# Optimization experiments

Hardware: AMD Instinct MI355X
Metric: run time of the kernel (lower is better)

Reference implementation:

```python
import jax, jax.numpy as jnp
import numpy as np

NUM_HEADS = 4
SCALE = 0.17677669529663687  # head_dim**-0.5, head_dim=32


def setup_inputs() -> dict:
    key = jax.random.key(0)
    k1, k2 = jax.random.split(key)
    qkv = jax.random.normal(k1, (2048, 144, 384), dtype=jnp.float32)
    mask = jax.random.normal(k2, (1, NUM_HEADS, 144, 144), dtype=jnp.float32)
    return {"qkv": qkv, "mask": mask}


def reference(qkv, mask):
    B, N, C = qkv.shape
    head_dim = C // NUM_HEADS // 3
    # [B,N,3,H,d] -> [3,B,H,N,d]
    qkv = qkv.reshape(B, N, 3, NUM_HEADS, head_dim).transpose(2, 0, 3, 1, 4)
    q, k, v = qkv[0], qkv[1], qkv[2]
    q = q * SCALE
    attn = jnp.einsum('bhnd,bhmd->bhnm', q, k) + mask  # mask broadcasts over B
    attn = jax.nn.softmax(attn, axis=-1)
    out = jnp.einsum('bhnm,bhmd->bhnd', attn, v)  # [B,H,N,d]
    return out.transpose(0, 2, 1, 3).reshape(B, N, C // 3)
```

## Files before the change

### kernel.cpp

```cpp
#include <hip/hip_runtime.h>


using short8 = __attribute__((ext_vector_type(8))) short;
using f32x4  = __attribute__((ext_vector_type(4))) float;

#define SEQ   144
#define NH    4
#define HD    32
#define C3    384
#define OC    128

#define KSTR  56
#define VSTR  168
#define PSTR  168

#define LOG2E 1.4426950408889634f
#define SCALE 0.17677669529663687f

__device__ __forceinline__ unsigned short f2bf(float f) {
  unsigned int u = __float_as_uint(f);
  u += 0x7fffu + ((u >> 16) & 1u);
  return (unsigned short)(u >> 16);
}

__global__ __launch_bounds__(256, 3)
void attn_kernel(const float* __restrict__ qkv,
                 const float* __restrict__ mask,
                 float* __restrict__ out)
{
  __shared__ __align__(16) unsigned short sK [SEQ * KSTR];
  __shared__ __align__(16) unsigned short sVT[HD  * VSTR];
  __shared__ __align__(16) unsigned short sP [4][16 * PSTR];

  const int tid = threadIdx.x;
  const int bid = blockIdx.x;
  const int b = bid >> 2;
  const int h = bid & 3;

  const float* qbase = qkv + (size_t)b * (SEQ * C3) + h * HD;
  const float* kbase = qbase + NH * HD;
  const float* vbase = qbase + 2 * NH * HD;

  {
    const int n0 = tid >> 4;
    const int d2 = (tid & 15) * 2;
    for (int p = 0; p < 9; ++p) {
      int n = p * 16 + n0;
      float2 kv = *(const float2*)(kbase + (size_t)n * C3 + d2);
      unsigned int pk = (unsigned int)f2bf(kv.x) | ((unsigned int)f2bf(kv.y) << 16);
      *(unsigned int*)&sK[n * KSTR + d2] = pk;
    }
  }
  {
    const int d  = tid & 31;
    const int n0 = tid >> 5;
    for (int p = 0; p < 18; ++p) {
      int n = p * 8 + n0;
      float v = vbase[(size_t)n * C3 + d];
      sVT[d * VSTR + n] = f2bf(v);
    }
    const int r  = tid >> 3;
    const int c0 = tid & 7;
    for (int p = 0; p < 3; ++p)
      sVT[r * VSTR + 144 + c0 + p * 8] = 0;
  }
  __syncthreads();

  const int lane = tid & 63;
  const int wv   = tid >> 6;
  const int m    = lane & 15;
  const int quad = lane >> 4;

  unsigned short* pbuf = sP[wv];
  for (int i = 0; i < 4; ++i) {
    int e = lane * 4 + i;
    pbuf[(e >> 4) * PSTR + 144 + (e & 15)] = 0;
  }

  const float qs = SCALE * LOG2E;
  const float* mbase = mask + (size_t)h * SEQ * SEQ;

  for (int s = wv; s < 9; s += 4) {
    short8 afrag;
    {
      const float* qrow = qbase + (size_t)(s * 16 + m) * C3 + quad * 8;
      float4 q0 = *(const float4*)(qrow);
      float4 q1 = *(const float4*)(qrow + 4);
      afrag[0] = (short)f2bf(q0.x * qs); afrag[1] = (short)f2bf(q0.y * qs);
      afrag[2] = (short)f2bf(q0.z * qs); afrag[3] = (short)f2bf(q0.w * qs);
      afrag[4] = (short)f2bf(q1.x * qs); afrag[5] = (short)f2bf(q1.y * qs);
      afrag[6] = (short)f2bf(q1.z * qs); afrag[7] = (short)f2bf(q1.w * qs);
    }

    float S[9][4];
    for (int nt = 0; nt < 9; ++nt) {
      f32x4 c = {0.f, 0.f, 0.f, 0.f};
      short8 bfrag = *(const short8*)&sK[(nt * 16 + m) * KSTR + quad * 8];
      c = __builtin_amdgcn_mfma_f32_16x16x32_bf16(afrag, bfrag, c, 0, 0, 0);
      const float* mrow = mbase + (size_t)(s * 16 + quad * 4) * SEQ + nt * 16 + m;
      S[nt][0] = c[0] + mrow[0 * SEQ] * LOG2E;
      S[nt][1] = c[1] + mrow[1 * SEQ] * LOG2E;
      S[nt][2] = c[2] + mrow[2 * SEQ] * LOG2E;
      S[nt][3] = c[3] + mrow[3 * SEQ] * LOG2E;
    }

    float mx[4], l[4];
    for (int r = 0; r < 4; ++r) {
      float v = S[0][r];
      for (int nt = 1; nt < 9; ++nt) v = fmaxf(v, S[nt][r]);
      v = fmaxf(v, __shfl_xor(v, 1));
      v = fmaxf(v, __shfl_xor(v, 2));
      v = fmaxf(v, __shfl_xor(v, 4));
      v = fmaxf(v, __shfl_xor(v, 8));
      mx[r] = v;
      l[r] = 0.f;
    }
    for (int nt = 0; nt < 9; ++nt)
      for (int r = 0; r < 4; ++r) {
        float p = __builtin_amdgcn_exp2f(S[nt][r] - mx[r]);
        S[nt][r] = p;
        l[r] += p;
      }
    for (int r = 0; r < 4; ++r) {
      float v = l[r];
      v += __shfl_xor(v, 1);
      v += __shfl_xor(v, 2);
      v += __shfl_xor(v, 4);
      v += __shfl_xor(v, 8);
      l[r] = 1.0f / v;
    }

    for (int nt = 0; nt < 9; ++nt)
      for (int r = 0; r < 4; ++r)
        pbuf[(quad * 4 + r) * PSTR + nt * 16 + m] = f2bf(S[nt][r]);

    f32x4 acc0 = {0.f, 0.f, 0.f, 0.f}, acc1 = {0.f, 0.f, 0.f, 0.f};
    for (int kt = 0; kt < 5; ++kt) {
      short8 pa = *(const short8*)&pbuf[m * PSTR + kt * 32 + quad * 8];
      short8 b0 = *(const short8*)&sVT[(m)      * VSTR + kt * 32 + quad * 8];
      short8 b1 = *(const short8*)&sVT[(16 + m) * VSTR + kt * 32 + quad * 8];
      acc0 = __builtin_amdgcn_mfma_f32_16x16x32_bf16(pa, b0, acc0, 0, 0, 0);
      acc1 = __builtin_amdgcn_mfma_f32_16x16x32_bf16(pa, b1, acc1, 0, 0, 0);
    }

    float* orow = out + ((size_t)b * SEQ + s * 16 + quad * 4) * OC + h * HD + m;
    for (int r = 0; r < 4; ++r) {
      orow[r * OC]      = acc0[r] * l[r];
      orow[r * OC + 16] = acc1[r] * l[r];
    }
  }
}

extern "C" void kernel_launch(void* const* d_in, const int* in_sizes, int n_in,
                              void* d_out, int out_size, void* d_ws, size_t ws_size,
                              hipStream_t stream) {
  const float* qkv  = (const float*)d_in[0];
  const float* mask = (const float*)d_in[1];
  float* out = (float*)d_out;
  attn_kernel<<<dim3(2048 * NH), dim3(256), 0, stream>>>(qkv, mask, out);
}
```

Measured before the change: 653.2 us.

## Vectorize K/V staging, prescale mask, swap PV operands for float4 stores

Loads K and V as float4 in one combined staging loop and packs bf16 with the library conversion. Q fragments are loaded before the staging barrier. A small pre-kernel multiplies the mask by log2e into the workspace, so it can serve directly as the MFMA accumulator init. The PV product now has V as the A operand, which makes each lane own contiguous output columns and allows float4 stores. It also trims the padded K tile with a half-masked final MFMA, shrinks LDS strides, and raises launch bounds to 4 blocks per CU. The cost is an extra kernel launch and different LDS bank patterns from the new strides.

```diff
diff --git a/kernel.cpp b/kernel.cpp
--- a/kernel.cpp
+++ b/kernel.cpp
@@ -1,4 +1,5 @@
 #include <hip/hip_runtime.h>
+#include <hip/hip_bf16.h>
 
 
 using short8 = __attribute__((ext_vector_type(8))) short;
@@ -10,9 +11,9 @@
 #define C3    384
 #define OC    128
 
-#define KSTR  56
-#define VSTR  168
-#define PSTR  168
+#define KSTR  40
+#define VSTR  152
+#define PSTR  152
 
 #define LOG2E 1.4426950408889634f
 #define SCALE 0.17677669529663687f
@@ -22,15 +23,25 @@
   u += 0x7fffu + ((u >> 16) & 1u);
   return (unsigned short)(u >> 16);
 }
-
-__global__ __launch_bounds__(256, 3)
+__device__ __forceinline__ unsigned int pkbf(float a, float b) {
+  __hip_bfloat162 h = __float22bfloat162_rn(make_float2(a, b));
+  union { __hip_bfloat162 h2; unsigned int u; } cv; cv.h2 = h;
+  return cv.u;
+}
+
+__global__ void mask_prep(const float* __restrict__ mask, float* __restrict__ o) {
+  int i = blockIdx.x * 256 + threadIdx.x;
+  o[i] = mask[i] * LOG2E;
+}
+
+__global__ __launch_bounds__(256, 4)
 void attn_kernel(const float* __restrict__ qkv,
-                 const float* __restrict__ mask,
+                 const float* __restrict__ maskS,
                  float* __restrict__ out)
 {
+  __shared__ __align__(16) unsigned short sP [4 * 16 * PSTR];
+  __shared__ __align__(16) unsigned short sVT[HD * VSTR];
   __shared__ __align__(16) unsigned short sK [SEQ * KSTR];
-  __shared__ __align__(16) unsigned short sVT[HD  * VSTR];
-  __shared__ __align__(16) unsigned short sP [4][16 * PSTR];
 
   const int tid = threadIdx.x;
   const int bid = blockIdx.x;
@@ -41,112 +52,147 @@
   const float* kbase = qbase + NH * HD;
   const float* vbase = qbase + 2 * NH * HD;
 
-  {
-    const int n0 = tid >> 4;
-    const int d2 = (tid & 15) * 2;
-    for (int p = 0; p < 9; ++p) {
-      int n = p * 16 + n0;
-      float2 kv = *(const float2*)(kbase + (size_t)n * C3 + d2);
-      unsigned int pk = (unsigned int)f2bf(kv.x) | ((unsigned int)f2bf(kv.y) << 16);
-      *(unsigned int*)&sK[n * KSTR + d2] = pk;
-    }
-  }
-  {
-    const int d  = tid & 31;
-    const int n0 = tid >> 5;
-    for (int p = 0; p < 18; ++p) {
-      int n = p * 8 + n0;
-      float v = vbase[(size_t)n * C3 + d];
-      sVT[d * VSTR + n] = f2bf(v);
-    }
-    const int r  = tid >> 3;
-    const int c0 = tid & 7;
-    for (int p = 0; p < 3; ++p)
-      sVT[r * VSTR + 144 + c0 + p * 8] = 0;
-  }
-  __syncthreads();
-
   const int lane = tid & 63;
   const int wv   = tid >> 6;
   const int m    = lane & 15;
   const int quad = lane >> 4;
 
-  unsigned short* pbuf = sP[wv];
-  for (int i = 0; i < 4; ++i) {
-    int e = lane * 4 + i;
-    pbuf[(e >> 4) * PSTR + 144 + (e & 15)] = 0;
-  }
-
   const float qs = SCALE * LOG2E;
-  const float* mbase = mask + (size_t)h * SEQ * SEQ;
-
-  for (int s = wv; s < 9; s += 4) {
-    short8 afrag;
-    {
+  float4 q0[3], q1[3];
+#pragma unroll
+  for (int i = 0; i < 3; ++i) {
+    int s = wv + 4 * i;
+    if (s < 9) {
       const float* qrow = qbase + (size_t)(s * 16 + m) * C3 + quad * 8;
-      float4 q0 = *(const float4*)(qrow);
-      float4 q1 = *(const float4*)(qrow + 4);
-      afrag[0] = (short)f2bf(q0.x * qs); afrag[1] = (short)f2bf(q0.y * qs);
-      afrag[2] = (short)f2bf(q0.z * qs); afrag[3] = (short)f2bf(q0.w * qs);
-      afrag[4] = (short)f2bf(q1.x * qs); afrag[5] = (short)f2bf(q1.y * qs);
-      afrag[6] = (short)f2bf(q1.z * qs); afrag[7] = (short)f2bf(q1.w * qs);
+      q0[i] = *(const float4*)(qrow);
+      q1[i] = *(const float4*)(qrow + 4);
     }
-
-    float S[9][4];
-    for (int nt = 0; nt < 9; ++nt) {
-      f32x4 c = {0.f, 0.f, 0.f, 0.f};
-      short8 bfrag = *(const short8*)&sK[(nt * 16 + m) * KSTR + quad * 8];
-      c = __builtin_amdgcn_mfma_f32_16x16x32_bf16(afrag, bfrag, c, 0, 0, 0);
-      const float* mrow = mbase + (size_t)(s * 16 + quad * 4) * SEQ + nt * 16 + m;
-      S[nt][0] = c[0] + mrow[0 * SEQ] * LOG2E;
-      S[nt][1] = c[1] + mrow[1 * SEQ] * LOG2E;
-      S[nt][2] = c[2] + mrow[2 * SEQ] * LOG2E;
-      S[nt][3] = c[3] + mrow[3 * SEQ] * LOG2E;
-    }
-
-    float mx[4], l[4];
-    for (int r = 0; r < 4; ++r) {
-      float v = S[0][r];
-      for (int nt = 1; nt < 9; ++nt) v = fmaxf(v, S[nt][r]);
-      v = fmaxf(v, __shfl_xor(v, 1));
-      v = fmaxf(v, __shfl_xor(v, 2));
-      v = fmaxf(v, __shfl_xor(v, 4));
-      v = fmaxf(v, __shfl_xor(v, 8));
-      mx[r] = v;
-      l[r] = 0.f;
-    }
-    for (int nt = 0; nt < 9; ++nt)
+  }
+
+  const int nr = tid >> 3;
+  const int d4 = (tid & 7) * 4;
+#pragma unroll
+  for (int p = 0; p < 4; ++p) {
+    int n = p * 32 + nr;
+    float4 k4 = *(const float4*)(kbase + (size_t)n * C3 + d4);
+    unsigned long long w = (unsigned long long)pkbf(k4.x, k4.y)
+                         | ((unsigned long long)pkbf(k4.z, k4.w) << 32);
+    *(unsigned long long*)&sK[n * KSTR + d4] = w;
+    float4 v4 = *(const float4*)(vbase + (size_t)n * C3 + d4);
+    sVT[(d4 + 0) * VSTR + n] = f2bf(v4.x);
+    sVT[(d4 + 1) * VSTR + n] = f2bf(v4.y);
+    sVT[(d4 + 2) * VSTR + n] = f2bf(v4.z);
+    sVT[(d4 + 3) * VSTR + n] = f2bf(v4.w);
+  }
+  if (nr < 16) {
+    int n = 128 + nr;
+    float4 k4 = *(const float4*)(kbase + (size_t)n * C3 + d4);
+    unsigned long long w = (unsigned long long)pkbf(k4.x, k4.y)
+                         | ((unsigned long long)pkbf(k4.z, k4.w) << 32);
+    *(unsigned long long*)&sK[n * KSTR + d4] = w;
+    float4 v4 = *(const float4*)(vbase + (size_t)n * C3 + d4);
+    sVT[(d4 + 0) * VSTR + n] = f2bf(v4.x);
+    sVT[(d4 + 1) * VSTR + n] = f2bf(v4.y);
+    sVT[(d4 + 2) * VSTR + n] = f2bf(v4.z);
+    sVT[(d4 + 3) * VSTR + n] = f2bf(v4.w);
+  }
+  __syncthreads();
+
+  unsigned short* pbuf = sP + wv * (16 * PSTR);
+  const float* mb = maskS + (size_t)h * SEQ * SEQ;
+
+#pragma unroll
+  for (int i = 0; i < 3; ++i) {
+    int s = wv + 4 * i;
+    if (s < 9) {
+      union { short8 s8; unsigned int u[4]; } af;
+      af.u[0] = pkbf(q0[i].x * qs, q0[i].y * qs);
+      af.u[1] = pkbf(q0[i].z * qs, q0[i].w * qs);
+      af.u[2] = pkbf(q1[i].x * qs, q1[i].y * qs);
+      af.u[3] = pkbf(q1[i].z * qs, q1[i].w * qs);
+
+      float S[9][4];
+      const float* mrow0 = mb + (size_t)(s * 16 + quad * 4) * SEQ + m;
+#pragma unroll
+      for (int nt = 0; nt < 9; ++nt) {
+        const float* mr = mrow0 + nt * 16;
+        f32x4 c;
+        c[0] = mr[0]; c[1] = mr[SEQ]; c[2] = mr[2 * SEQ]; c[3] = mr[3 * SEQ];
+        short8 bfrag = *(const short8*)&sK[(nt * 16 + m) * KSTR + quad * 8];
+        c = __builtin_amdgcn_mfma_f32_16x16x32_bf16(af.s8, bfrag, c, 0, 0, 0);
+        S[nt][0] = c[0]; S[nt][1] = c[1]; S[nt][2] = c[2]; S[nt][3] = c[3];
+      }
+
+      float mx[4], l[4];
+#pragma unroll
       for (int r = 0; r < 4; ++r) {
-        float p = __builtin_amdgcn_exp2f(S[nt][r] - mx[r]);
-        S[nt][r] = p;
-        l[r] += p;
-      }
-    for (int r = 0; r < 4; ++r) {
-      float v = l[r];
-      v += __shfl_xor(v, 1);
-      v += __shfl_xor(v, 2);
-      v += __shfl_xor(v, 4);
-      v += __shfl_xor(v, 8);
-      l[r] = 1.0f / v;
-    }
-
-    for (int nt = 0; nt < 9; ++nt)
-      for (int r = 0; r < 4; ++r)
-        pbuf[(quad * 4 + r) * PSTR + nt * 16 + m] = f2bf(S[nt][r]);
-
-    f32x4 acc0 = {0.f, 0.f, 0.f, 0.f}, acc1 = {0.f, 0.f, 0.f, 0.f};
-    for (int kt = 0; kt < 5; ++kt) {
-      short8 pa = *(const short8*)&pbuf[m * PSTR + kt * 32 + quad * 8];
-      short8 b0 = *(const short8*)&sVT[(m)      * VSTR + kt * 32 + quad * 8];
-      short8 b1 = *(const short8*)&sVT[(16 + m) * VSTR + kt * 32 + quad * 8];
-      acc0 = __builtin_amdgcn_mfma_f32_16x16x32_bf16(pa, b0, acc0, 0, 0, 0);
-      acc1 = __builtin_amdgcn_mfma_f32_16x16x32_bf16(pa, b1, acc1, 0, 0, 0);
-    }
-
-    float* orow = out + ((size_t)b * SEQ + s * 16 + quad * 4) * OC + h * HD + m;
-    for (int r = 0; r < 4; ++r) {
-      orow[r * OC]      = acc0[r] * l[r];
-      orow[r * OC + 16] = acc1[r] * l[r];
+        float a = fmaxf(fmaxf(S[0][r], S[1][r]), S[2][r]);
+        float bb = fmaxf(fmaxf(S[3][r], S[4][r]), S[5][r]);
+        float cc = fmaxf(fmaxf(S[6][r], S[7][r]), S[8][r]);
+        float v = fmaxf(fmaxf(a, bb), cc);
+        v = fmaxf(v, __shfl_xor(v, 1));
+        v = fmaxf(v, __shfl_xor(v, 2));
+        v = fmaxf(v, __shfl_xor(v, 4));
+        v = fmaxf(v, __shfl_xor(v, 8));
+        mx[r] = v; l[r] = 0.f;
+      }
+#pragma unroll
+      for (int nt = 0; nt < 9; ++nt)
+#pragma unroll
+        for (int r = 0; r < 4; ++r) {
+          float p = __builtin_amdgcn_exp2f(S[nt][r] - mx[r]);
+          S[nt][r] = p;
+          l[r] += p;
+        }
+#pragma unroll
+      for (int r = 0; r < 4; ++r) {
+        float v = l[r];
+        v += __shfl_xor(v, 1);
+        v += __shfl_xor(v, 2);
+        v += __shfl_xor(v, 4);
+        v += __shfl_xor(v, 8);
+        l[r] = v;
+      }
+      int src = (m >> 2) * 16 + m;
+      float s0 = __shfl(l[0], src), s1 = __shfl(l[1], src);
+      float s2 = __shfl(l[2], src), s3 = __shfl(l[3], src);
+      float lsel = (m & 2) ? ((m & 1) ? s3 : s2) : ((m & 1) ? s1 : s0);
+      float linv = __builtin_amdgcn_rcpf(lsel);
+
+#pragma unroll
+      for (int nt = 0; nt < 9; ++nt)
+#pragma unroll
+        for (int r = 0; r < 4; ++r)
+          pbuf[(quad * 4 + r) * PSTR + nt * 16 + m] = f2bf(S[nt][r]);
+
+      f32x4 acc0 = {0.f, 0.f, 0.f, 0.f}, acc1 = {0.f, 0.f, 0.f, 0.f};
+#pragma unroll
+      for (int kt = 0; kt < 4; ++kt) {
+        short8 pa  = *(const short8*)&pbuf[m * PSTR + kt * 32 + quad * 8];
+        short8 va0 = *(const short8*)&sVT[(m)      * VSTR + kt * 32 + quad * 8];
+        short8 va1 = *(const short8*)&sVT[(16 + m) * VSTR + kt * 32 + quad * 8];
+        acc0 = __builtin_amdgcn_mfma_f32_16x16x32_bf16(va0, pa, acc0, 0, 0, 0);
+        acc1 = __builtin_amdgcn_mfma_f32_16x16x32_bf16(va1, pa, acc1, 0, 0, 0);
+      }
+      {
+        int off = 128 + (quad & 1) * 8;
+        short8 z = {0, 0, 0, 0, 0, 0, 0, 0};
+        short8 pa  = *(const short8*)&pbuf[m * PSTR + off];
+        short8 va0 = *(const short8*)&sVT[(m)      * VSTR + off];
+        short8 va1 = *(const short8*)&sVT[(16 + m) * VSTR + off];
+        if (quad >= 2) { pa = z; va0 = z; va1 = z; }
+        acc0 = __builtin_amdgcn_mfma_f32_16x16x32_bf16(va0, pa, acc0, 0, 0, 0);
+        acc1 = __builtin_amdgcn_mfma_f32_16x16x32_bf16(va1, pa, acc1, 0, 0, 0);
+      }
+
+      float* orow = out + ((size_t)b * SEQ + s * 16 + m) * OC + h * HD + quad * 4;
+      float4 o0, o1;
+      o0.x = acc0[0] * linv; o0.y = acc0[1] * linv;
+      o0.z = acc0[2] * linv; o0.w = acc0[3] * linv;
+      o1.x = acc1[0] * linv; o1.y = acc1[1] * linv;
+      o1.z = acc1[2] * linv; o1.w = acc1[3] * linv;
+      *(float4*)(orow)      = o0;
+      *(float4*)(orow + 16) = o1;
     }
   }
 }
@@ -157,5 +203,7 @@
   const float* qkv  = (const float*)d_in[0];
   const float* mask = (const float*)d_in[1];
   float* out = (float*)d_out;
-  attn_kernel<<<dim3(2048 * NH), dim3(256), 0, stream>>>(qkv, mask, out);
-}
+  float* maskS = (float*)d_ws;
+  mask_prep<<<dim3(324), dim3(256), 0, stream>>>(mask, maskS);
+  attn_kernel<<<dim3(2048 * NH), dim3(256), 0, stream>>>(qkv, maskS, out);
+}
```

Result: no change. 653.9 us (+0.1%).
